# Kernel tuning notes

Hardware: AMD Instinct MI355X
Metric: run time of the kernel (lower is better)

Reference implementation:

```python
import jax, jax.numpy as jnp
import numpy as np

NCHW = ('NCHW', 'OIHW', 'NCHW')


def _conv3x3_same(x, w, b):
    # ZeroPad2d(1) + 3x3 valid conv == 3x3 conv with padding 1
    y = jax.lax.conv_general_dilated(x, w, window_strides=(1, 1),
                                     padding=((1, 1), (1, 1)),
                                     dimension_numbers=NCHW)
    return y + b[None, :, None, None]


def _maxpool2(x):
    return jax.lax.reduce_window(x, -jnp.inf, jax.lax.max,
                                 (1, 1, 2, 2), (1, 1, 2, 2), 'VALID')


def setup_inputs() -> dict:
    key = jax.random.key(0)
    ks = jax.random.split(key, 12)
    B, T1, T2, R, D = 1, 512, 512, 9, 3840
    q = jax.random.normal(ks[0], (B, T1, R, D), jnp.float32)
    t = jax.random.normal(ks[1], (B, T2, R, D), jnp.float32)
    # ViSiL features are L2-normalized region descriptors -> sims in [-1,1]
    q = q / jnp.linalg.norm(q, axis=-1, keepdims=True)
    t = t / jnp.linalg.norm(t, axis=-1, keepdims=True)
    s = 0.05
    return {
        'query': q, 'target': t,
        'w1': jax.random.normal(ks[2], (32, 1, 3, 3), jnp.float32) * s,
        'b1': jax.random.normal(ks[3], (32,), jnp.float32) * s,
        'w2': jax.random.normal(ks[4], (64, 32, 3, 3), jnp.float32) * s,
        'b2': jax.random.normal(ks[5], (64,), jnp.float32) * s,
        'w3': jax.random.normal(ks[6], (128, 64, 3, 3), jnp.float32) * s,
        'b3': jax.random.normal(ks[7], (128,), jnp.float32) * s,
        'wf': jax.random.normal(ks[8], (1, 128, 1, 1), jnp.float32) * s,
        'bf': jax.random.normal(ks[9], (1,), jnp.float32) * s,
    }


def reference(query, target, w1, b1, w2, b2, w3, b3, wf, bf):
    # frame-to-frame: region-pair similarity [B,T1,O,P,T2]
    sim5 = jnp.einsum('biok,bjpk->biopj', query, target)
    # Chamfer (axes=[3,2]): max over target regions P, mean over query regions O
    f2f = jnp.mean(jnp.max(sim5, axis=3), axis=2)  # [B,T1,T2]
    # video comperator CNN
    x = f2f[:, None]                                 # [B,1,T1,T2]
    x = _maxpool2(jax.nn.relu(_conv3x3_same(x, w1, b1)))
    x = _maxpool2(jax.nn.relu(_conv3x3_same(x, w2, b2)))
    x = jax.nn.relu(_conv3x3_same(x, w3, b3))
    x = jax.lax.conv_general_dilated(x, wf, (1, 1), ((0, 0), (0, 0)),
                                     dimension_numbers=NCHW)
    x = x + bf[None, :, None, None]
    s = jnp.clip(x[:, 0], -1.0, 1.0)                 # Hardtanh, [B,H,W]
    # video-to-video Chamfer (axes=[2,1]): max over axis 2, mean over axis 1
    return jnp.mean(jnp.max(s, axis=2), axis=1)      # [B]
```

## Files before the change

### kernel.cpp

```cpp
#include <hip/hip_runtime.h>
#include <hip/hip_bf16.h>

typedef float f32x4 __attribute__((ext_vector_type(4)));
typedef int v8i __attribute__((ext_vector_type(8)));

#define AS3 __attribute__((address_space(3)))
#define AS1 __attribute__((address_space(1)))

__global__ __launch_bounds__(256) void cvt_fp8_kernel(const float* __restrict__ q,
                                                      const float* __restrict__ t,
                                                      unsigned int* __restrict__ qd,
                                                      unsigned int* __restrict__ td) {
  int b = blockIdx.x;
  const float4* s4;
  unsigned int* dst;
  int base;
  if (b < 4320) { s4 = (const float4*)q; dst = qd; base = b * 1024; }
  else          { s4 = (const float4*)t; dst = td; base = (b - 4320) * 1024; }
#pragma unroll
  for (int i = 0; i < 4; ++i) {
    int j = base + i * 256 + threadIdx.x;
    float4 v = s4[j];
    int w = 0;
    w = __builtin_amdgcn_cvt_pk_fp8_f32(v.x * 16.f, v.y * 16.f, w, false);
    w = __builtin_amdgcn_cvt_pk_fp8_f32(v.z * 16.f, v.w * 16.f, w, true);
    dst[j] = w;
  }
}

__global__ __launch_bounds__(768) void gemm_cmax_kernel(const unsigned char* __restrict__ qf8,
                                                        const unsigned char* __restrict__ tf8,
                                                        float* __restrict__ f2f) {
  __shared__ __align__(16) char smem[147456];
  const int tid  = threadIdx.x;
  const int wv   = tid >> 6;
  const int lane = tid & 63;
  const int quad = lane >> 4;
  const int l16  = lane & 15;
  const int wrow = wv >> 1, wcol = wv & 1;
  const int x = blockIdx.x & 7, r = blockIdx.x >> 3;
  const int bi = (x >> 1) * 4 + (r & 3);
  const int bj = (x & 1) * 8 + (r >> 2);

  f32x4 acc[3][9];
#pragma unroll
  for (int a = 0; a < 3; ++a)
#pragma unroll
    for (int b = 0; b < 9; ++b) acc[a][b] = (f32x4){0.f, 0.f, 0.f, 0.f};

  const unsigned char* gptr[6];
#pragma unroll
  for (int i = 0; i < 6; ++i) {
    int s   = i * 768 + wv * 64 + lane;
    int mat = (s >= 2304);
    int sm  = s - mat * 2304;
    int row = sm >> 3, pc = sm & 7;
    int gc  = pc ^ (row & 7);
    const unsigned char* base = mat ? (tf8 + (size_t)(bj * 288 + row) * 3840)
                                    : (qf8 + (size_t)(bi * 288 + row) * 3840);
    gptr[i] = base + gc * 16;
  }

  int buf = 0;
#pragma unroll
  for (int i = 0; i < 6; ++i)
    __builtin_amdgcn_global_load_lds((const AS1 void*)(gptr[i]),
                                     (AS3 void*)(smem + (i * 768 + wv * 64) * 16), 16, 0, 0);

  const int arow0 = wrow * 48 + l16;
  const int bcol0 = wcol * 144 + l16;

  for (int kt = 0; kt < 30; ++kt) {
    __syncthreads();
    if (kt < 29) {
      int nb = buf ^ 1;
#pragma unroll
      for (int i = 0; i < 6; ++i)
        __builtin_amdgcn_global_load_lds((const AS1 void*)(gptr[i] + (kt + 1) * 128),
                                         (AS3 void*)(smem + nb * 73728 + (i * 768 + wv * 64) * 16),
                                         16, 0, 0);
    }
    const char* A = smem + buf * 73728;
    const char* B = A + 36864;

    v8i av[3];
#pragma unroll
    for (int sr = 0; sr < 3; ++sr) {
      int row = arow0 + sr * 16;
      int sw  = row & 7;
      int p0  = (quad * 2) ^ sw, p1 = (quad * 2 + 1) ^ sw;
      int4 lo = *(const int4*)(A + row * 128 + p0 * 16);
      int4 hi = *(const int4*)(A + row * 128 + p1 * 16);
      v8i v;
      v[0] = lo.x; v[1] = lo.y; v[2] = lo.z; v[3] = lo.w;
      v[4] = hi.x; v[5] = hi.y; v[6] = hi.z; v[7] = hi.w;
      av[sr] = v;
    }
#pragma unroll
    for (int c = 0; c < 9; ++c) {
      int col = bcol0 + c * 16;
      int sw  = col & 7;
      int p0  = (quad * 2) ^ sw, p1 = (quad * 2 + 1) ^ sw;
      int4 lo = *(const int4*)(B + col * 128 + p0 * 16);
      int4 hi = *(const int4*)(B + col * 128 + p1 * 16);
      v8i bv;
      bv[0] = lo.x; bv[1] = lo.y; bv[2] = lo.z; bv[3] = lo.w;
      bv[4] = hi.x; bv[5] = hi.y; bv[6] = hi.z; bv[7] = hi.w;
      acc[0][c] = __builtin_amdgcn_mfma_scale_f32_16x16x128_f8f6f4(
          av[0], bv, acc[0][c], 0, 0, 0, 0x7f7f7f7f, 0, 0x7f7f7f7f);
      acc[1][c] = __builtin_amdgcn_mfma_scale_f32_16x16x128_f8f6f4(
          av[1], bv, acc[1][c], 0, 0, 0, 0x7f7f7f7f, 0, 0x7f7f7f7f);
      acc[2][c] = __builtin_amdgcn_mfma_scale_f32_16x16x128_f8f6f4(
          av[2], bv, acc[2][c], 0, 0, 0, 0x7f7f7f7f, 0, 0x7f7f7f7f);
    }
    buf ^= 1;
  }

  __syncthreads();
  float* scr  = (float*)smem;
  float* mbuf = (float*)(smem + 18432);
#pragma unroll
  for (int b = 0; b < 18; ++b) {
    const int bw = b / 3, bs = b - bw * 3;
    if (wrow == bw) {
#pragma unroll
      for (int c = 0; c < 9; ++c)
#pragma unroll
        for (int rr = 0; rr < 4; ++rr)
          scr[(quad * 4 + rr) * 288 + wcol * 144 + c * 16 + l16] = acc[bs][c][rr] * (1.f / 256.f);
    }
    __syncthreads();
    if (tid < 512) {
      int row = tid >> 5, jg = tid & 31;
      const float* p = scr + row * 288 + jg * 9;
      float m = p[0];
#pragma unroll
      for (int k = 1; k < 9; ++k) m = fmaxf(m, p[k]);
      mbuf[(b * 16 + row) * 33 + jg] = m;
    }
    __syncthreads();
  }
  for (int p = tid; p < 1024; p += 768) {
    int il = p >> 5, jg = p & 31;
    const float* mp = mbuf + (il * 9) * 33 + jg;
    float s = 0.f;
#pragma unroll
    for (int o = 0; o < 9; ++o) s += mp[o * 33];
    f2f[(size_t)(bi * 32 + il) * 512 + bj * 32 + jg] = s * (1.f / 9.f);
  }
}

__global__ __launch_bounds__(256) void conv1_kernel(const float* __restrict__ in,
                                                    const float* __restrict__ w1,
                                                    const float* __restrict__ b1,
                                                    float* __restrict__ out) {
  __shared__ float tile[34 * 36];
  __shared__ float wl[320];
  int t = blockIdx.x & 255;
  int chg = blockIdx.x >> 8;
  int ty0 = (t >> 4) * 32, tx0 = (t & 15) * 32;
  int py = threadIdx.x >> 4, px = threadIdx.x & 15;

  for (int idx = threadIdx.x; idx < 320; idx += 256)
    wl[idx] = (idx < 288) ? w1[idx] : b1[idx - 288];
  for (int idx = threadIdx.x; idx < 34 * 34; idx += 256) {
    int r = idx / 34, c = idx % 34;
    int gy = ty0 + r - 1, gx = tx0 + c - 1;
    tile[r * 36 + c] = ((unsigned)gy < 512u && (unsigned)gx < 512u) ? in[gy * 512 + gx] : 0.f;
  }
  __syncthreads();

  float win[4][4];
#pragma unroll
  for (int r = 0; r < 4; ++r)
#pragma unroll
    for (int c = 0; c < 4; ++c)
      win[r][c] = tile[(2 * py + r) * 36 + 2 * px + c];

  int gy2 = (t >> 4) * 16 + py, gx2 = (t & 15) * 16 + px;
  int ch0 = chg * 8;
  for (int ch = ch0; ch < ch0 + 8; ++ch) {
    float w[9];
#pragma unroll
    for (int k = 0; k < 9; ++k) w[k] = wl[ch * 9 + k];
    float m = -INFINITY;
#pragma unroll
    for (int a = 0; a < 2; ++a)
#pragma unroll
      for (int b = 0; b < 2; ++b) {
        float s = 0.f;
#pragma unroll
        for (int ky = 0; ky < 3; ++ky)
#pragma unroll
          for (int kx = 0; kx < 3; ++kx) s += win[a + ky][b + kx] * w[ky * 3 + kx];
        m = fmaxf(m, s);
      }
    out[ch * 65536 + gy2 * 256 + gx2] = fmaxf(m + wl[288 + ch], 0.f);
  }
}

__global__ __launch_bounds__(256) void conv2_kernel(const float* __restrict__ in,
                                                    const float* __restrict__ w2,
                                                    const float* __restrict__ b2,
                                                    float* __restrict__ out) {
  __shared__ __align__(16) float wlds[32 * 4 * 12];
  __shared__ __align__(16) float tile[2 * 2 * 10 * 264];
  const int tid = threadIdx.x;
  const int stripe = blockIdx.x & 31, cog = blockIdx.x >> 5;
  const int X = tid;
  const int Y0 = stripe * 8;

  for (int idx = tid; idx < 1152; idx += 256) {
    int co = idx / 288, rem = idx % 288, ci = rem / 9, k = rem % 9;
    wlds[(ci * 4 + co) * 12 + k] = w2[((cog * 4 + co) * 32 + ci) * 9 + k];
  }
  if (tid < 80) {
    int bu = tid / 40, rem = tid % 40, pl = rem / 20, r2 = rem % 20;
    int rr = r2 >> 1, side = r2 & 1;
    tile[bu * 5280 + pl * 2640 + rr * 264 + (side ? 260 : 3)] = 0.f;
  }
  int gof[5], lof[5];
#pragma unroll
  for (int i = 0; i < 5; ++i) {
    int idx = tid + i * 256;
    int rw = idx >> 6, c4 = idx & 63;
    int pl = (rw >= 10), rr = rw - pl * 10;
    int gy = Y0 + rr - 1;
    lof[i] = pl * 2640 + rr * 264 + 4 + c4 * 4;
    gof[i] = ((unsigned)gy < 256u) ? (pl * 65536 + gy * 256 + c4 * 4) : -1;
  }
#pragma unroll
  for (int i = 0; i < 5; ++i) {
    float4 v = (gof[i] >= 0) ? *(const float4*)(in + gof[i]) : (float4){0, 0, 0, 0};
    *(float4*)&tile[lof[i]] = v;
  }
  __syncthreads();

  float acc[8][4];
#pragma unroll
  for (int y = 0; y < 8; ++y)
#pragma unroll
    for (int co = 0; co < 4; ++co) acc[y][co] = 0.f;

#pragma unroll 1
  for (int cb = 0; cb < 16; ++cb) {
    int buf = cb & 1;
    float4 pf[5];
    if (cb < 15) {
#pragma unroll
      for (int i = 0; i < 5; ++i)
        pf[i] = (gof[i] >= 0) ? *(const float4*)(in + gof[i] + (cb + 1) * 131072)
                              : (float4){0, 0, 0, 0};
    }
    const float* tb = tile + buf * 5280;
#pragma unroll
    for (int pl = 0; pl < 2; ++pl) {
      const float* tp = tb + pl * 2640;
      int ci = cb * 2 + pl;
      float w[4][9];
#pragma unroll
      for (int co = 0; co < 4; ++co) {
        const float* wp = &wlds[(ci * 4 + co) * 12];
        float4 w0 = *(const float4*)wp;
        float4 w1 = *(const float4*)(wp + 4);
        w[co][0] = w0.x; w[co][1] = w0.y; w[co][2] = w0.z; w[co][3] = w0.w;
        w[co][4] = w1.x; w[co][5] = w1.y; w[co][6] = w1.z; w[co][7] = w1.w;
        w[co][8] = wp[8];
      }
      float r0[3], r1[3], r2[3];
      const float* p0 = tp + X + 3;
      r0[0] = p0[0]; r0[1] = p0[1]; r0[2] = p0[2];
      const float* p1 = tp + 264 + X + 3;
      r1[0] = p1[0]; r1[1] = p1[1]; r1[2] = p1[2];
#pragma unroll
      for (int y = 0; y < 8; ++y) {
        const float* p2 = tp + (y + 2) * 264 + X + 3;
        r2[0] = p2[0]; r2[1] = p2[1]; r2[2] = p2[2];
#pragma unroll
        for (int co = 0; co < 4; ++co)
          acc[y][co] += r0[0] * w[co][0] + r0[1] * w[co][1] + r0[2] * w[co][2]
                      + r1[0] * w[co][3] + r1[1] * w[co][4] + r1[2] * w[co][5]
                      + r2[0] * w[co][6] + r2[1] * w[co][7] + r2[2] * w[co][8];
        r0[0] = r1[0]; r0[1] = r1[1]; r0[2] = r1[2];
        r1[0] = r2[0]; r1[1] = r2[1]; r1[2] = r2[2];
      }
    }
    if (cb < 15) {
#pragma unroll
      for (int i = 0; i < 5; ++i)
        *(float4*)&tile[(buf ^ 1) * 5280 + lof[i]] = pf[i];
    }
    __syncthreads();
  }

  int x2 = X >> 1;
#pragma unroll
  for (int co = 0; co < 4; ++co) {
    float bias = b2[cog * 4 + co];
#pragma unroll
    for (int y2 = 0; y2 < 4; ++y2) {
      float v = fmaxf(acc[2 * y2][co], acc[2 * y2 + 1][co]);
      v = fmaxf(v + bias, 0.f);
      float o = fmaxf(v, __shfl_xor(v, 1, 64));
      if ((X & 1) == 0)
        out[(cog * 4 + co) * 16384 + (stripe * 4 + y2) * 128 + x2] = o;
    }
  }
}

__global__ __launch_bounds__(256) void conv3_kernel(const float* __restrict__ in,
                                                    const float* __restrict__ w3,
                                                    const float* __restrict__ b3,
                                                    float* __restrict__ out) {
  __shared__ __align__(16) float wlds[64 * 2 * 12];
  __shared__ __align__(16) float tile[2 * 2 * 18 * 136];
  const int tid = threadIdx.x;
  const int stripe = blockIdx.x & 7, cog = blockIdx.x >> 3;
  const int X = tid & 127, yh = tid >> 7;
  const int Y0 = stripe * 16;

  for (int idx = tid; idx < 1152; idx += 256) {
    int co = idx / 576, rem = idx % 576, ci = rem / 9, k = rem % 9;
    wlds[(ci * 2 + co) * 12 + k] = w3[((cog * 2 + co) * 64 + ci) * 9 + k];
  }
  if (tid < 144) {
    int bu = tid / 72, rem = tid % 72, pl = rem / 36, r2 = rem % 36;
    int rr = r2 >> 1, side = r2 & 1;
    tile[bu * 4896 + pl * 2448 + rr * 136 + (side ? 132 : 3)] = 0.f;
  }
  int gof[5], lof[5];
#pragma unroll
  for (int i = 0; i < 5; ++i) {
    int idx = tid + i * 256;
    if (idx < 1152) {
      int rw = idx >> 5, c4 = idx & 31;
      int pl = (rw >= 18), rr = rw - pl * 18;
      int gy = Y0 + rr - 1;
      lof[i] = pl * 2448 + rr * 136 + 4 + c4 * 4;
      gof[i] = ((unsigned)gy < 128u) ? (pl * 16384 + gy * 128 + c4 * 4) : -1;
    } else { lof[i] = -1; gof[i] = -1; }
  }
#pragma unroll
  for (int i = 0; i < 5; ++i)
    if (lof[i] >= 0) {
      float4 v = (gof[i] >= 0) ? *(const float4*)(in + gof[i]) : (float4){0, 0, 0, 0};
      *(float4*)&tile[lof[i]] = v;
    }
  __syncthreads();

  float acc[8][2];
#pragma unroll
  for (int y = 0; y < 8; ++y)
#pragma unroll
    for (int co = 0; co < 2; ++co) acc[y][co] = 0.f;

#pragma unroll 1
  for (int cb = 0; cb < 32; ++cb) {
    int buf = cb & 1;
    float4 pf[5];
    if (cb < 31) {
#pragma unroll
      for (int i = 0; i < 5; ++i)
        pf[i] = (gof[i] >= 0) ? *(const float4*)(in + gof[i] + (cb + 1) * 32768)
                              : (float4){0, 0, 0, 0};
    }
    const float* tb = tile + buf * 4896;
#pragma unroll
    for (int pl = 0; pl < 2; ++pl) {
      const float* tp = tb + pl * 2448;
      int ci = cb * 2 + pl;
      float w[2][9];
#pragma unroll
      for (int co = 0; co < 2; ++co) {
        const float* wp = &wlds[(ci * 2 + co) * 12];
        float4 w0 = *(const float4*)wp;
        float4 w1 = *(const float4*)(wp + 4);
        w[co][0] = w0.x; w[co][1] = w0.y; w[co][2] = w0.z; w[co][3] = w0.w;
        w[co][4] = w1.x; w[co][5] = w1.y; w[co][6] = w1.z; w[co][7] = w1.w;
        w[co][8] = wp[8];
      }
      float r0[3], r1[3], r2[3];
      const float* p0 = tp + (yh * 8) * 136 + X + 3;
      r0[0] = p0[0]; r0[1] = p0[1]; r0[2] = p0[2];
      const float* p1 = tp + (yh * 8 + 1) * 136 + X + 3;
      r1[0] = p1[0]; r1[1] = p1[1]; r1[2] = p1[2];
#pragma unroll
      for (int y = 0; y < 8; ++y) {
        const float* p2 = tp + (yh * 8 + y + 2) * 136 + X + 3;
        r2[0] = p2[0]; r2[1] = p2[1]; r2[2] = p2[2];
#pragma unroll
        for (int co = 0; co < 2; ++co)
          acc[y][co] += r0[0] * w[co][0] + r0[1] * w[co][1] + r0[2] * w[co][2]
                      + r1[0] * w[co][3] + r1[1] * w[co][4] + r1[2] * w[co][5]
                      + r2[0] * w[co][6] + r2[1] * w[co][7] + r2[2] * w[co][8];
        r0[0] = r1[0]; r0[1] = r1[1]; r0[2] = r1[2];
        r1[0] = r2[0]; r1[1] = r2[1]; r1[2] = r2[2];
      }
    }
    if (cb < 31) {
#pragma unroll
      for (int i = 0; i < 5; ++i)
        if (lof[i] >= 0) *(float4*)&tile[(buf ^ 1) * 4896 + lof[i]] = pf[i];
    }
    __syncthreads();
  }

#pragma unroll
  for (int co = 0; co < 2; ++co) {
    float bias = b3[cog * 2 + co];
    float* op = out + (cog * 2 + co) * 16384 + (Y0 + yh * 8) * 128 + X;
#pragma unroll
    for (int y = 0; y < 8; ++y)
      op[y * 128] = fmaxf(acc[y][co] + bias, 0.f);
  }
}

__global__ __launch_bounds__(512) void convf_kernel(const float* __restrict__ in,
                                                    const float* __restrict__ wf,
                                                    const float* __restrict__ bfp,
                                                    float* __restrict__ rowm) {
  __shared__ float part[512];
  int y = blockIdx.x, tid = threadIdx.x;
  int pt = tid >> 7, x = tid & 127;
  float acc = 0.f;
  const float* ip = in + y * 128 + x;
  for (int ci = pt * 32; ci < pt * 32 + 32; ++ci) acc += ip[ci * 16384] * wf[ci];
  part[tid] = acc;
  __syncthreads();
  if (tid < 128) {
    float s = part[tid] + part[tid + 128] + part[tid + 256] + part[tid + 384] + bfp[0];
    part[tid] = fminf(fmaxf(s, -1.f), 1.f);
  }
  __syncthreads();
  if (tid < 64) {
    float m = fmaxf(part[tid], part[tid + 64]);
    for (int off = 32; off; off >>= 1) m = fmaxf(m, __shfl_down(m, off, 64));
    if (tid == 0) rowm[y] = m;
  }
}

__global__ __launch_bounds__(128) void final_kernel(const float* __restrict__ rowm,
                                                    float* __restrict__ out) {
  int x = threadIdx.x;
  float v = rowm[x];
  for (int off = 32; off; off >>= 1) v += __shfl_down(v, off, 64);
  __shared__ float red[2];
  if ((x & 63) == 0) red[x >> 6] = v;
  __syncthreads();
  if (x == 0) out[0] = (red[0] + red[1]) * (1.f / 128.f);
}

extern "C" void kernel_launch(void* const* d_in, const int* in_sizes, int n_in,
                              void* d_out, int out_size, void* d_ws, size_t ws_size,
                              hipStream_t stream) {
  const float* q  = (const float*)d_in[0];
  const float* t  = (const float*)d_in[1];
  const float* w1 = (const float*)d_in[2];
  const float* b1 = (const float*)d_in[3];
  const float* w2 = (const float*)d_in[4];
  const float* b2 = (const float*)d_in[5];
  const float* w3 = (const float*)d_in[6];
  const float* b3 = (const float*)d_in[7];
  const float* wf = (const float*)d_in[8];
  const float* bf = (const float*)d_in[9];
  float* out = (float*)d_out;
  char* ws = (char*)d_ws;

  unsigned char* qf8 = (unsigned char*)(ws + 0);
  unsigned char* tf8 = (unsigned char*)(ws + 17694720);
  float* f2f  = (float*)(ws + 44826624);
  float* x1   = (float*)(ws + 45875200);
  float* x2b  = (float*)(ws + 54263808);
  float* x3   = (float*)(ws + 58458112);
  float* rowm = (float*)(ws + 66846720);

  cvt_fp8_kernel<<<8640, 256, 0, stream>>>(q, t, (unsigned int*)qf8, (unsigned int*)tf8);
  gemm_cmax_kernel<<<256, 768, 0, stream>>>(qf8, tf8, f2f);
  conv1_kernel<<<1024, 256, 0, stream>>>(f2f, w1, b1, x1);
  conv2_kernel<<<512, 256, 0, stream>>>(x1, w2, b2, x2b);
  conv3_kernel<<<512, 256, 0, stream>>>(x2b, w3, b3, x3);
  convf_kernel<<<128, 512, 0, stream>>>(x3, wf, bf, rowm);
  final_kernel<<<1, 128, 0, stream>>>(rowm, out);
}
```

Before: 384.4 us.

## Fuse conv stages into one persistent kernel with grid barriers

Replaces the five separate conv/reduction kernel launches with a single 512-block kernel that runs conv1, conv2, conv3, the 1x1 conv and the final reduction in sequence. Stages are separated by atomic-counter grid barriers, and the counters are reset with a memset before each run. The goal is to remove launch gaps and tail effects between the small conv kernels. The cost is spin-wait barrier overhead, and it relies on all 512 blocks being co-resident, which holds given the shared-memory and thread usage on this GPU.

```diff
diff --git a/kernel.cpp b/kernel.cpp
--- a/kernel.cpp
+++ b/kernel.cpp
@@ -150,304 +150,325 @@
   }
 }
 
-__global__ __launch_bounds__(256) void conv1_kernel(const float* __restrict__ in,
-                                                    const float* __restrict__ w1,
-                                                    const float* __restrict__ b1,
-                                                    float* __restrict__ out) {
-  __shared__ float tile[34 * 36];
-  __shared__ float wl[320];
-  int t = blockIdx.x & 255;
-  int chg = blockIdx.x >> 8;
-  int ty0 = (t >> 4) * 32, tx0 = (t & 15) * 32;
-  int py = threadIdx.x >> 4, px = threadIdx.x & 15;
-
-  for (int idx = threadIdx.x; idx < 320; idx += 256)
-    wl[idx] = (idx < 288) ? w1[idx] : b1[idx - 288];
-  for (int idx = threadIdx.x; idx < 34 * 34; idx += 256) {
-    int r = idx / 34, c = idx % 34;
-    int gy = ty0 + r - 1, gx = tx0 + c - 1;
-    tile[r * 36 + c] = ((unsigned)gy < 512u && (unsigned)gx < 512u) ? in[gy * 512 + gx] : 0.f;
-  }
+__device__ __forceinline__ void grid_barrier(unsigned int* cnt, unsigned int nb) {
   __syncthreads();
-
-  float win[4][4];
-#pragma unroll
-  for (int r = 0; r < 4; ++r)
-#pragma unroll
-    for (int c = 0; c < 4; ++c)
-      win[r][c] = tile[(2 * py + r) * 36 + 2 * px + c];
-
-  int gy2 = (t >> 4) * 16 + py, gx2 = (t & 15) * 16 + px;
-  int ch0 = chg * 8;
-  for (int ch = ch0; ch < ch0 + 8; ++ch) {
-    float w[9];
-#pragma unroll
-    for (int k = 0; k < 9; ++k) w[k] = wl[ch * 9 + k];
-    float m = -INFINITY;
-#pragma unroll
-    for (int a = 0; a < 2; ++a)
-#pragma unroll
-      for (int b = 0; b < 2; ++b) {
-        float s = 0.f;
-#pragma unroll
-        for (int ky = 0; ky < 3; ++ky)
-#pragma unroll
-          for (int kx = 0; kx < 3; ++kx) s += win[a + ky][b + kx] * w[ky * 3 + kx];
-        m = fmaxf(m, s);
-      }
-    out[ch * 65536 + gy2 * 256 + gx2] = fmaxf(m + wl[288 + ch], 0.f);
-  }
+  if (threadIdx.x == 0) {
+    __threadfence();
+    atomicAdd(cnt, 1u);
+    while (atomicAdd(cnt, 0u) < nb) __builtin_amdgcn_s_sleep(8);
+    __threadfence();
+  }
+  __syncthreads();
 }
 
-__global__ __launch_bounds__(256) void conv2_kernel(const float* __restrict__ in,
-                                                    const float* __restrict__ w2,
-                                                    const float* __restrict__ b2,
-                                                    float* __restrict__ out) {
-  __shared__ __align__(16) float wlds[32 * 4 * 12];
-  __shared__ __align__(16) float tile[2 * 2 * 10 * 264];
+__global__ __launch_bounds__(256) void megaconv_kernel(const float* __restrict__ f2f,
+                                                       const float* __restrict__ w1,
+                                                       const float* __restrict__ b1,
+                                                       const float* __restrict__ w2,
+                                                       const float* __restrict__ b2,
+                                                       const float* __restrict__ w3,
+                                                       const float* __restrict__ b3,
+                                                       const float* __restrict__ wf,
+                                                       const float* __restrict__ bfp,
+                                                       float* __restrict__ x1,
+                                                       float* __restrict__ x2b,
+                                                       float* __restrict__ x3,
+                                                       float* __restrict__ rowm,
+                                                       unsigned int* __restrict__ bars,
+                                                       float* __restrict__ out) {
+  __shared__ __align__(16) char pool[48384];
+  const int b = blockIdx.x;
   const int tid = threadIdx.x;
-  const int stripe = blockIdx.x & 31, cog = blockIdx.x >> 5;
-  const int X = tid;
-  const int Y0 = stripe * 8;
-
-  for (int idx = tid; idx < 1152; idx += 256) {
-    int co = idx / 288, rem = idx % 288, ci = rem / 9, k = rem % 9;
-    wlds[(ci * 4 + co) * 12 + k] = w2[((cog * 4 + co) * 32 + ci) * 9 + k];
-  }
-  if (tid < 80) {
-    int bu = tid / 40, rem = tid % 40, pl = rem / 20, r2 = rem % 20;
-    int rr = r2 >> 1, side = r2 & 1;
-    tile[bu * 5280 + pl * 2640 + rr * 264 + (side ? 260 : 3)] = 0.f;
-  }
-  int gof[5], lof[5];
-#pragma unroll
-  for (int i = 0; i < 5; ++i) {
-    int idx = tid + i * 256;
-    int rw = idx >> 6, c4 = idx & 63;
-    int pl = (rw >= 10), rr = rw - pl * 10;
-    int gy = Y0 + rr - 1;
-    lof[i] = pl * 2640 + rr * 264 + 4 + c4 * 4;
-    gof[i] = ((unsigned)gy < 256u) ? (pl * 65536 + gy * 256 + c4 * 4) : -1;
-  }
-#pragma unroll
-  for (int i = 0; i < 5; ++i) {
-    float4 v = (gof[i] >= 0) ? *(const float4*)(in + gof[i]) : (float4){0, 0, 0, 0};
-    *(float4*)&tile[lof[i]] = v;
-  }
-  __syncthreads();
-
-  float acc[8][4];
-#pragma unroll
-  for (int y = 0; y < 8; ++y)
-#pragma unroll
-    for (int co = 0; co < 4; ++co) acc[y][co] = 0.f;
-
+
+  {
+    float* wl = (float*)pool;
+    float* tile1 = (float*)(pool + 1280);
+    int t = b & 255;
+    int ty0 = (t >> 4) * 32, tx0 = (t & 15) * 32;
+    int py = tid >> 4, px = tid & 15;
+
+    for (int idx = tid; idx < 320; idx += 256)
+      wl[idx] = (idx < 288) ? w1[idx] : b1[idx - 288];
+    for (int idx = tid; idx < 34 * 34; idx += 256) {
+      int rr = idx / 34, cc = idx % 34;
+      int gy = ty0 + rr - 1, gx = tx0 + cc - 1;
+      tile1[rr * 36 + cc] = ((unsigned)gy < 512u && (unsigned)gx < 512u) ? f2f[gy * 512 + gx] : 0.f;
+    }
+    __syncthreads();
+
+    float win[4][4];
+#pragma unroll
+    for (int rr = 0; rr < 4; ++rr)
+#pragma unroll
+      for (int cc = 0; cc < 4; ++cc)
+        win[rr][cc] = tile1[(2 * py + rr) * 36 + 2 * px + cc];
+
+    int gy2 = (t >> 4) * 16 + py, gx2 = (t & 15) * 16 + px;
 #pragma unroll 1
-  for (int cb = 0; cb < 16; ++cb) {
-    int buf = cb & 1;
-    float4 pf[5];
-    if (cb < 15) {
-#pragma unroll
-      for (int i = 0; i < 5; ++i)
-        pf[i] = (gof[i] >= 0) ? *(const float4*)(in + gof[i] + (cb + 1) * 131072)
-                              : (float4){0, 0, 0, 0};
-    }
-    const float* tb = tile + buf * 5280;
-#pragma unroll
-    for (int pl = 0; pl < 2; ++pl) {
-      const float* tp = tb + pl * 2640;
-      int ci = cb * 2 + pl;
-      float w[4][9];
-#pragma unroll
-      for (int co = 0; co < 4; ++co) {
-        const float* wp = &wlds[(ci * 4 + co) * 12];
-        float4 w0 = *(const float4*)wp;
-        float4 w1 = *(const float4*)(wp + 4);
-        w[co][0] = w0.x; w[co][1] = w0.y; w[co][2] = w0.z; w[co][3] = w0.w;
-        w[co][4] = w1.x; w[co][5] = w1.y; w[co][6] = w1.z; w[co][7] = w1.w;
-        w[co][8] = wp[8];
-      }
-      float r0[3], r1[3], r2[3];
-      const float* p0 = tp + X + 3;
-      r0[0] = p0[0]; r0[1] = p0[1]; r0[2] = p0[2];
-      const float* p1 = tp + 264 + X + 3;
-      r1[0] = p1[0]; r1[1] = p1[1]; r1[2] = p1[2];
-#pragma unroll
-      for (int y = 0; y < 8; ++y) {
-        const float* p2 = tp + (y + 2) * 264 + X + 3;
-        r2[0] = p2[0]; r2[1] = p2[1]; r2[2] = p2[2];
-#pragma unroll
-        for (int co = 0; co < 4; ++co)
-          acc[y][co] += r0[0] * w[co][0] + r0[1] * w[co][1] + r0[2] * w[co][2]
-                      + r1[0] * w[co][3] + r1[1] * w[co][4] + r1[2] * w[co][5]
-                      + r2[0] * w[co][6] + r2[1] * w[co][7] + r2[2] * w[co][8];
-        r0[0] = r1[0]; r0[1] = r1[1]; r0[2] = r1[2];
-        r1[0] = r2[0]; r1[1] = r2[1]; r1[2] = r2[2];
-      }
-    }
-    if (cb < 15) {
-#pragma unroll
-      for (int i = 0; i < 5; ++i)
-        *(float4*)&tile[(buf ^ 1) * 5280 + lof[i]] = pf[i];
-    }
-    __syncthreads();
-  }
-
-  int x2 = X >> 1;
-#pragma unroll
-  for (int co = 0; co < 4; ++co) {
-    float bias = b2[cog * 4 + co];
-#pragma unroll
-    for (int y2 = 0; y2 < 4; ++y2) {
-      float v = fmaxf(acc[2 * y2][co], acc[2 * y2 + 1][co]);
-      v = fmaxf(v + bias, 0.f);
-      float o = fmaxf(v, __shfl_xor(v, 1, 64));
-      if ((X & 1) == 0)
-        out[(cog * 4 + co) * 16384 + (stripe * 4 + y2) * 128 + x2] = o;
-    }
-  }
-}
-
-__global__ __launch_bounds__(256) void conv3_kernel(const float* __restrict__ in,
-                                                    const float* __restrict__ w3,
-                                                    const float* __restrict__ b3,
-                                                    float* __restrict__ out) {
-  __shared__ __align__(16) float wlds[64 * 2 * 12];
-  __shared__ __align__(16) float tile[2 * 2 * 18 * 136];
-  const int tid = threadIdx.x;
-  const int stripe = blockIdx.x & 7, cog = blockIdx.x >> 3;
-  const int X = tid & 127, yh = tid >> 7;
-  const int Y0 = stripe * 16;
-
-  for (int idx = tid; idx < 1152; idx += 256) {
-    int co = idx / 576, rem = idx % 576, ci = rem / 9, k = rem % 9;
-    wlds[(ci * 2 + co) * 12 + k] = w3[((cog * 2 + co) * 64 + ci) * 9 + k];
-  }
-  if (tid < 144) {
-    int bu = tid / 72, rem = tid % 72, pl = rem / 36, r2 = rem % 36;
-    int rr = r2 >> 1, side = r2 & 1;
-    tile[bu * 4896 + pl * 2448 + rr * 136 + (side ? 132 : 3)] = 0.f;
-  }
-  int gof[5], lof[5];
-#pragma unroll
-  for (int i = 0; i < 5; ++i) {
-    int idx = tid + i * 256;
-    if (idx < 1152) {
-      int rw = idx >> 5, c4 = idx & 31;
-      int pl = (rw >= 18), rr = rw - pl * 18;
+    for (int g = 0; g < 2; ++g) {
+      int ch0 = ((b >> 8) + g * 2) * 8;
+      for (int ch = ch0; ch < ch0 + 8; ++ch) {
+        float w[9];
+#pragma unroll
+        for (int k = 0; k < 9; ++k) w[k] = wl[ch * 9 + k];
+        float m = -INFINITY;
+#pragma unroll
+        for (int a = 0; a < 2; ++a)
+#pragma unroll
+          for (int bb = 0; bb < 2; ++bb) {
+            float s = 0.f;
+#pragma unroll
+            for (int ky = 0; ky < 3; ++ky)
+#pragma unroll
+              for (int kx = 0; kx < 3; ++kx) s += win[a + ky][bb + kx] * w[ky * 3 + kx];
+            m = fmaxf(m, s);
+          }
+        x1[ch * 65536 + gy2 * 256 + gx2] = fmaxf(m + wl[288 + ch], 0.f);
+      }
+    }
+  }
+  grid_barrier(bars + 0, 512);
+
+  {
+    float* wlds = (float*)pool;
+    float* tile = (float*)(pool + 6144);
+    const int stripe = b & 31, cog = b >> 5;
+    const int X = tid;
+    const int Y0 = stripe * 8;
+
+    for (int idx = tid; idx < 1152; idx += 256) {
+      int co = idx / 288, rem = idx % 288, ci = rem / 9, k = rem % 9;
+      wlds[(ci * 4 + co) * 12 + k] = w2[((cog * 4 + co) * 32 + ci) * 9 + k];
+    }
+    if (tid < 80) {
+      int bu = tid / 40, rem = tid % 40, pl = rem / 20, r2 = rem % 20;
+      int rr = r2 >> 1, side = r2 & 1;
+      tile[bu * 5280 + pl * 2640 + rr * 264 + (side ? 260 : 3)] = 0.f;
+    }
+    int gof[5], lof[5];
+#pragma unroll
+    for (int i = 0; i < 5; ++i) {
+      int idx = tid + i * 256;
+      int rw = idx >> 6, c4 = idx & 63;
+      int pl = (rw >= 10), rr = rw - pl * 10;
       int gy = Y0 + rr - 1;
-      lof[i] = pl * 2448 + rr * 136 + 4 + c4 * 4;
-      gof[i] = ((unsigned)gy < 128u) ? (pl * 16384 + gy * 128 + c4 * 4) : -1;
-    } else { lof[i] = -1; gof[i] = -1; }
-  }
-#pragma unroll
-  for (int i = 0; i < 5; ++i)
-    if (lof[i] >= 0) {
-      float4 v = (gof[i] >= 0) ? *(const float4*)(in + gof[i]) : (float4){0, 0, 0, 0};
+      lof[i] = pl * 2640 + rr * 264 + 4 + c4 * 4;
+      gof[i] = ((unsigned)gy < 256u) ? (pl * 65536 + gy * 256 + c4 * 4) : -1;
+    }
+#pragma unroll
+    for (int i = 0; i < 5; ++i) {
+      float4 v = (gof[i] >= 0) ? *(const float4*)(x1 + gof[i]) : (float4){0, 0, 0, 0};
       *(float4*)&tile[lof[i]] = v;
     }
-  __syncthreads();
-
-  float acc[8][2];
-#pragma unroll
-  for (int y = 0; y < 8; ++y)
-#pragma unroll
-    for (int co = 0; co < 2; ++co) acc[y][co] = 0.f;
+    __syncthreads();
+
+    float acc[8][4];
+#pragma unroll
+    for (int y = 0; y < 8; ++y)
+#pragma unroll
+      for (int co = 0; co < 4; ++co) acc[y][co] = 0.f;
 
 #pragma unroll 1
-  for (int cb = 0; cb < 32; ++cb) {
-    int buf = cb & 1;
-    float4 pf[5];
-    if (cb < 31) {
-#pragma unroll
-      for (int i = 0; i < 5; ++i)
-        pf[i] = (gof[i] >= 0) ? *(const float4*)(in + gof[i] + (cb + 1) * 32768)
-                              : (float4){0, 0, 0, 0};
-    }
-    const float* tb = tile + buf * 4896;
-#pragma unroll
-    for (int pl = 0; pl < 2; ++pl) {
-      const float* tp = tb + pl * 2448;
-      int ci = cb * 2 + pl;
-      float w[2][9];
-#pragma unroll
-      for (int co = 0; co < 2; ++co) {
-        const float* wp = &wlds[(ci * 2 + co) * 12];
-        float4 w0 = *(const float4*)wp;
-        float4 w1 = *(const float4*)(wp + 4);
-        w[co][0] = w0.x; w[co][1] = w0.y; w[co][2] = w0.z; w[co][3] = w0.w;
-        w[co][4] = w1.x; w[co][5] = w1.y; w[co][6] = w1.z; w[co][7] = w1.w;
-        w[co][8] = wp[8];
-      }
-      float r0[3], r1[3], r2[3];
-      const float* p0 = tp + (yh * 8) * 136 + X + 3;
-      r0[0] = p0[0]; r0[1] = p0[1]; r0[2] = p0[2];
-      const float* p1 = tp + (yh * 8 + 1) * 136 + X + 3;
-      r1[0] = p1[0]; r1[1] = p1[1]; r1[2] = p1[2];
-#pragma unroll
-      for (int y = 0; y < 8; ++y) {
-        const float* p2 = tp + (yh * 8 + y + 2) * 136 + X + 3;
-        r2[0] = p2[0]; r2[1] = p2[1]; r2[2] = p2[2];
-#pragma unroll
-        for (int co = 0; co < 2; ++co)
-          acc[y][co] += r0[0] * w[co][0] + r0[1] * w[co][1] + r0[2] * w[co][2]
-                      + r1[0] * w[co][3] + r1[1] * w[co][4] + r1[2] * w[co][5]
-                      + r2[0] * w[co][6] + r2[1] * w[co][7] + r2[2] * w[co][8];
-        r0[0] = r1[0]; r0[1] = r1[1]; r0[2] = r1[2];
-        r1[0] = r2[0]; r1[1] = r2[1]; r1[2] = r2[2];
-      }
-    }
-    if (cb < 31) {
-#pragma unroll
-      for (int i = 0; i < 5; ++i)
-        if (lof[i] >= 0) *(float4*)&tile[(buf ^ 1) * 4896 + lof[i]] = pf[i];
-    }
-    __syncthreads();
-  }
-
-#pragma unroll
-  for (int co = 0; co < 2; ++co) {
-    float bias = b3[cog * 2 + co];
-    float* op = out + (cog * 2 + co) * 16384 + (Y0 + yh * 8) * 128 + X;
+    for (int cb = 0; cb < 16; ++cb) {
+      int buf = cb & 1;
+      float4 pf[5];
+      if (cb < 15) {
+#pragma unroll
+        for (int i = 0; i < 5; ++i)
+          pf[i] = (gof[i] >= 0) ? *(const float4*)(x1 + gof[i] + (cb + 1) * 131072)
+                                : (float4){0, 0, 0, 0};
+      }
+      const float* tb = tile + buf * 5280;
+#pragma unroll
+      for (int pl = 0; pl < 2; ++pl) {
+        const float* tp = tb + pl * 2640;
+        int ci = cb * 2 + pl;
+        float w[4][9];
+#pragma unroll
+        for (int co = 0; co < 4; ++co) {
+          const float* wp = &wlds[(ci * 4 + co) * 12];
+          float4 w0 = *(const float4*)wp;
+          float4 w1v = *(const float4*)(wp + 4);
+          w[co][0] = w0.x; w[co][1] = w0.y; w[co][2] = w0.z; w[co][3] = w0.w;
+          w[co][4] = w1v.x; w[co][5] = w1v.y; w[co][6] = w1v.z; w[co][7] = w1v.w;
+          w[co][8] = wp[8];
+        }
+        float r0[3], r1[3], r2[3];
+        const float* p0 = tp + X + 3;
+        r0[0] = p0[0]; r0[1] = p0[1]; r0[2] = p0[2];
+        const float* p1 = tp + 264 + X + 3;
+        r1[0] = p1[0]; r1[1] = p1[1]; r1[2] = p1[2];
+#pragma unroll
+        for (int y = 0; y < 8; ++y) {
+          const float* p2 = tp + (y + 2) * 264 + X + 3;
+          r2[0] = p2[0]; r2[1] = p2[1]; r2[2] = p2[2];
+#pragma unroll
+          for (int co = 0; co < 4; ++co)
+            acc[y][co] += r0[0] * w[co][0] + r0[1] * w[co][1] + r0[2] * w[co][2]
+                        + r1[0] * w[co][3] + r1[1] * w[co][4] + r1[2] * w[co][5]
+                        + r2[0] * w[co][6] + r2[1] * w[co][7] + r2[2] * w[co][8];
+          r0[0] = r1[0]; r0[1] = r1[1]; r0[2] = r1[2];
+          r1[0] = r2[0]; r1[1] = r2[1]; r1[2] = r2[2];
+        }
+      }
+      if (cb < 15) {
+#pragma unroll
+        for (int i = 0; i < 5; ++i)
+          *(float4*)&tile[(buf ^ 1) * 5280 + lof[i]] = pf[i];
+      }
+      __syncthreads();
+    }
+
+    int x2 = X >> 1;
+#pragma unroll
+    for (int co = 0; co < 4; ++co) {
+      float bias = b2[cog * 4 + co];
+#pragma unroll
+      for (int y2 = 0; y2 < 4; ++y2) {
+        float v = fmaxf(acc[2 * y2][co], acc[2 * y2 + 1][co]);
+        v = fmaxf(v + bias, 0.f);
+        float o = fmaxf(v, __shfl_xor(v, 1, 64));
+        if ((X & 1) == 0)
+          x2b[(cog * 4 + co) * 16384 + (stripe * 4 + y2) * 128 + x2] = o;
+      }
+    }
+  }
+  grid_barrier(bars + 1, 512);
+
+  {
+    float* wlds = (float*)pool;
+    float* tile = (float*)(pool + 6144);
+    const int stripe = b & 7, cog = b >> 3;
+    const int X = tid & 127, yh = tid >> 7;
+    const int Y0 = stripe * 16;
+
+    for (int idx = tid; idx < 1152; idx += 256) {
+      int co = idx / 576, rem = idx % 576, ci = rem / 9, k = rem % 9;
+      wlds[(ci * 2 + co) * 12 + k] = w3[((cog * 2 + co) * 64 + ci) * 9 + k];
+    }
+    if (tid < 144) {
+      int bu = tid / 72, rem = tid % 72, pl = rem / 36, r2 = rem % 36;
+      int rr = r2 >> 1, side = r2 & 1;
+      tile[bu * 4896 + pl * 2448 + rr * 136 + (side ? 132 : 3)] = 0.f;
+    }
+    int gof[5], lof[5];
+#pragma unroll
+    for (int i = 0; i < 5; ++i) {
+      int idx = tid + i * 256;
+      if (idx < 1152) {
+        int rw = idx >> 5, c4 = idx & 31;
+        int pl = (rw >= 18), rr = rw - pl * 18;
+        int gy = Y0 + rr - 1;
+        lof[i] = pl * 2448 + rr * 136 + 4 + c4 * 4;
+        gof[i] = ((unsigned)gy < 128u) ? (pl * 16384 + gy * 128 + c4 * 4) : -1;
+      } else { lof[i] = -1; gof[i] = -1; }
+    }
+#pragma unroll
+    for (int i = 0; i < 5; ++i)
+      if (lof[i] >= 0) {
+        float4 v = (gof[i] >= 0) ? *(const float4*)(x2b + gof[i]) : (float4){0, 0, 0, 0};
+        *(float4*)&tile[lof[i]] = v;
+      }
+    __syncthreads();
+
+    float acc[8][2];
 #pragma unroll
     for (int y = 0; y < 8; ++y)
-      op[y * 128] = fmaxf(acc[y][co] + bias, 0.f);
-  }
-}
-
-__global__ __launch_bounds__(512) void convf_kernel(const float* __restrict__ in,
-                                                    const float* __restrict__ wf,
-                                                    const float* __restrict__ bfp,
-                                                    float* __restrict__ rowm) {
-  __shared__ float part[512];
-  int y = blockIdx.x, tid = threadIdx.x;
-  int pt = tid >> 7, x = tid & 127;
-  float acc = 0.f;
-  const float* ip = in + y * 128 + x;
-  for (int ci = pt * 32; ci < pt * 32 + 32; ++ci) acc += ip[ci * 16384] * wf[ci];
-  part[tid] = acc;
-  __syncthreads();
-  if (tid < 128) {
-    float s = part[tid] + part[tid + 128] + part[tid + 256] + part[tid + 384] + bfp[0];
-    part[tid] = fminf(fmaxf(s, -1.f), 1.f);
-  }
-  __syncthreads();
-  if (tid < 64) {
-    float m = fmaxf(part[tid], part[tid + 64]);
-    for (int off = 32; off; off >>= 1) m = fmaxf(m, __shfl_down(m, off, 64));
-    if (tid == 0) rowm[y] = m;
-  }
-}
-
-__global__ __launch_bounds__(128) void final_kernel(const float* __restrict__ rowm,
-                                                    float* __restrict__ out) {
-  int x = threadIdx.x;
-  float v = rowm[x];
-  for (int off = 32; off; off >>= 1) v += __shfl_down(v, off, 64);
-  __shared__ float red[2];
-  if ((x & 63) == 0) red[x >> 6] = v;
-  __syncthreads();
-  if (x == 0) out[0] = (red[0] + red[1]) * (1.f / 128.f);
+#pragma unroll
+      for (int co = 0; co < 2; ++co) acc[y][co] = 0.f;
+
+#pragma unroll 1
+    for (int cb = 0; cb < 32; ++cb) {
+      int buf = cb & 1;
+      float4 pf[5];
+      if (cb < 31) {
+#pragma unroll
+        for (int i = 0; i < 5; ++i)
+          pf[i] = (gof[i] >= 0) ? *(const float4*)(x2b + gof[i] + (cb + 1) * 32768)
+                                : (float4){0, 0, 0, 0};
+      }
+      const float* tb = tile + buf * 4896;
+#pragma unroll
+      for (int pl = 0; pl < 2; ++pl) {
+        const float* tp = tb + pl * 2448;
+        int ci = cb * 2 + pl;
+        float w[2][9];
+#pragma unroll
+        for (int co = 0; co < 2; ++co) {
+          const float* wp = &wlds[(ci * 2 + co) * 12];
+          float4 w0 = *(const float4*)wp;
+          float4 w1v = *(const float4*)(wp + 4);
+          w[co][0] = w0.x; w[co][1] = w0.y; w[co][2] = w0.z; w[co][3] = w0.w;
+          w[co][4] = w1v.x; w[co][5] = w1v.y; w[co][6] = w1v.z; w[co][7] = w1v.w;
+          w[co][8] = wp[8];
+        }
+        float r0[3], r1[3], r2[3];
+        const float* p0 = tp + (yh * 8) * 136 + X + 3;
+        r0[0] = p0[0]; r0[1] = p0[1]; r0[2] = p0[2];
+        const float* p1 = tp + (yh * 8 + 1) * 136 + X + 3;
+        r1[0] = p1[0]; r1[1] = p1[1]; r1[2] = p1[2];
+#pragma unroll
+        for (int y = 0; y < 8; ++y) {
+          const float* p2 = tp + (yh * 8 + y + 2) * 136 + X + 3;
+          r2[0] = p2[0]; r2[1] = p2[1]; r2[2] = p2[2];
+#pragma unroll
+          for (int co = 0; co < 2; ++co)
+            acc[y][co] += r0[0] * w[co][0] + r0[1] * w[co][1] + r0[2] * w[co][2]
+                        + r1[0] * w[co][3] + r1[1] * w[co][4] + r1[2] * w[co][5]
+                        + r2[0] * w[co][6] + r2[1] * w[co][7] + r2[2] * w[co][8];
+          r0[0] = r1[0]; r0[1] = r1[1]; r0[2] = r1[2];
+          r1[0] = r2[0]; r1[1] = r2[1]; r1[2] = r2[2];
+        }
+      }
+      if (cb < 31) {
+#pragma unroll
+        for (int i = 0; i < 5; ++i)
+          if (lof[i] >= 0) *(float4*)&tile[(buf ^ 1) * 4896 + lof[i]] = pf[i];
+      }
+      __syncthreads();
+    }
+
+#pragma unroll
+    for (int co = 0; co < 2; ++co) {
+      float bias = b3[cog * 2 + co];
+      float* op = x3 + (cog * 2 + co) * 16384 + (Y0 + yh * 8) * 128 + X;
+#pragma unroll
+      for (int y = 0; y < 8; ++y)
+        op[y * 128] = fmaxf(acc[y][co] + bias, 0.f);
+    }
+  }
+  grid_barrier(bars + 2, 512);
+
+  if (b < 128) {
+    float* fpart = (float*)pool;
+    int y = b;
+    int xx = tid & 127, pt = tid >> 7;
+    float acc = 0.f;
+    const float* ip = x3 + y * 128 + xx;
+    for (int ci = pt * 64; ci < pt * 64 + 64; ++ci) acc += ip[ci * 16384] * wf[ci];
+    fpart[tid] = acc;
+    __syncthreads();
+    if (tid < 128) {
+      float s = fpart[tid] + fpart[tid + 128] + bfp[0];
+      fpart[tid] = fminf(fmaxf(s, -1.f), 1.f);
+    }
+    __syncthreads();
+    if (tid < 64) {
+      float m = fmaxf(fpart[tid], fpart[tid + 64]);
+      for (int off = 32; off; off >>= 1) m = fmaxf(m, __shfl_down(m, off, 64));
+      if (tid == 0) rowm[y] = m;
+    }
+  }
+  grid_barrier(bars + 3, 512);
+
+  if (b == 0) {
+    float* red = (float*)pool;
+    float v = (tid < 128) ? rowm[tid] : 0.f;
+    for (int off = 32; off; off >>= 1) v += __shfl_down(v, off, 64);
+    if (tid < 128 && (tid & 63) == 0) red[tid >> 6] = v;
+    __syncthreads();
+    if (tid == 0) out[0] = (red[0] + red[1]) * (1.f / 128.f);
+  }
 }
 
 extern "C" void kernel_launch(void* const* d_in, const int* in_sizes, int n_in,
@@ -473,12 +494,11 @@
   float* x2b  = (float*)(ws + 54263808);
   float* x3   = (float*)(ws + 58458112);
   float* rowm = (float*)(ws + 66846720);
-
+  unsigned int* bars = (unsigned int*)(ws + 66847232);
+
+  hipMemsetAsync(bars, 0, 64, stream);
   cvt_fp8_kernel<<<8640, 256, 0, stream>>>(q, t, (unsigned int*)qf8, (unsigned int*)tf8);
   gemm_cmax_kernel<<<256, 768, 0, stream>>>(qf8, tf8, f2f);
-  conv1_kernel<<<1024, 256, 0, stream>>>(f2f, w1, b1, x1);
-  conv2_kernel<<<512, 256, 0, stream>>>(x1, w2, b2, x2b);
-  conv3_kernel<<<512, 256, 0, stream>>>(x2b, w3, b3, x3);
-  convf_kernel<<<128, 512, 0, stream>>>(x3, wf, bf, rowm);
-  final_kernel<<<1, 128, 0, stream>>>(rowm, out);
+  megaconv_kernel<<<512, 256, 0, stream>>>(f2f, w1, b1, w2, b2, w3, b3, wf, bf,
+                                           x1, x2b, x3, rowm, bars, out);
 }
```

Measured after the change: 545.8 us. +42.0%, slower.

## Fuse conv3, final 1x1 conv and reduction via grid barrier

Applied to the files above, without the earlier changes.

Merges conv3, the 1x1 conv with row-max, and the final mean into one kernel. After conv3 a device-wide atomic barrier waits for all 512 blocks, then 128 blocks compute the row maxima and the last block to finish does the mean. This removes two kernel launches and their gaps, at the cost of an added memset and a spin barrier. The barrier assumes all 512 blocks are resident at once; if they are not, the kernel deadlocks.

```diff
diff --git a/kernel.cpp b/kernel.cpp
--- a/kernel.cpp
+++ b/kernel.cpp
@@ -262,9 +262,9 @@
       for (int co = 0; co < 4; ++co) {
         const float* wp = &wlds[(ci * 4 + co) * 12];
         float4 w0 = *(const float4*)wp;
-        float4 w1 = *(const float4*)(wp + 4);
+        float4 w1v = *(const float4*)(wp + 4);
         w[co][0] = w0.x; w[co][1] = w0.y; w[co][2] = w0.z; w[co][3] = w0.w;
-        w[co][4] = w1.x; w[co][5] = w1.y; w[co][6] = w1.z; w[co][7] = w1.w;
+        w[co][4] = w1v.x; w[co][5] = w1v.y; w[co][6] = w1v.z; w[co][7] = w1v.w;
         w[co][8] = wp[8];
       }
       float r0[3], r1[3], r2[3];
@@ -308,14 +308,21 @@
   }
 }
 
-__global__ __launch_bounds__(256) void conv3_kernel(const float* __restrict__ in,
-                                                    const float* __restrict__ w3,
-                                                    const float* __restrict__ b3,
-                                                    float* __restrict__ out) {
+__global__ __launch_bounds__(256) void conv3f_kernel(const float* __restrict__ in,
+                                                     const float* __restrict__ w3,
+                                                     const float* __restrict__ b3,
+                                                     const float* __restrict__ wf,
+                                                     const float* __restrict__ bfp,
+                                                     float* __restrict__ x3,
+                                                     float* __restrict__ rowm,
+                                                     unsigned int* __restrict__ bars,
+                                                     float* __restrict__ out) {
   __shared__ __align__(16) float wlds[64 * 2 * 12];
   __shared__ __align__(16) float tile[2 * 2 * 18 * 136];
+  __shared__ unsigned int lastf;
+  const int b = blockIdx.x;
   const int tid = threadIdx.x;
-  const int stripe = blockIdx.x & 7, cog = blockIdx.x >> 3;
+  const int stripe = b & 7, cog = b >> 3;
   const int X = tid & 127, yh = tid >> 7;
   const int Y0 = stripe * 16;
 
@@ -374,9 +381,9 @@
       for (int co = 0; co < 2; ++co) {
         const float* wp = &wlds[(ci * 2 + co) * 12];
         float4 w0 = *(const float4*)wp;
-        float4 w1 = *(const float4*)(wp + 4);
+        float4 w1v = *(const float4*)(wp + 4);
         w[co][0] = w0.x; w[co][1] = w0.y; w[co][2] = w0.z; w[co][3] = w0.w;
-        w[co][4] = w1.x; w[co][5] = w1.y; w[co][6] = w1.z; w[co][7] = w1.w;
+        w[co][4] = w1v.x; w[co][5] = w1v.y; w[co][6] = w1v.z; w[co][7] = w1v.w;
         w[co][8] = wp[8];
       }
       float r0[3], r1[3], r2[3];
@@ -408,46 +415,59 @@
 #pragma unroll
   for (int co = 0; co < 2; ++co) {
     float bias = b3[cog * 2 + co];
-    float* op = out + (cog * 2 + co) * 16384 + (Y0 + yh * 8) * 128 + X;
+    float* op = x3 + (cog * 2 + co) * 16384 + (Y0 + yh * 8) * 128 + X;
 #pragma unroll
     for (int y = 0; y < 8; ++y)
       op[y * 128] = fmaxf(acc[y][co] + bias, 0.f);
   }
-}
-
-__global__ __launch_bounds__(512) void convf_kernel(const float* __restrict__ in,
-                                                    const float* __restrict__ wf,
-                                                    const float* __restrict__ bfp,
-                                                    float* __restrict__ rowm) {
-  __shared__ float part[512];
-  int y = blockIdx.x, tid = threadIdx.x;
-  int pt = tid >> 7, x = tid & 127;
-  float acc = 0.f;
-  const float* ip = in + y * 128 + x;
-  for (int ci = pt * 32; ci < pt * 32 + 32; ++ci) acc += ip[ci * 16384] * wf[ci];
-  part[tid] = acc;
+
   __syncthreads();
-  if (tid < 128) {
-    float s = part[tid] + part[tid + 128] + part[tid + 256] + part[tid + 384] + bfp[0];
-    part[tid] = fminf(fmaxf(s, -1.f), 1.f);
+  if (tid == 0) {
+    __threadfence();
+    __hip_atomic_fetch_add(bars + 0, 1u, __ATOMIC_ACQ_REL, __HIP_MEMORY_SCOPE_AGENT);
+    while (__hip_atomic_load(bars + 0, __ATOMIC_ACQUIRE, __HIP_MEMORY_SCOPE_AGENT) < 512u)
+      __builtin_amdgcn_s_sleep(32);
+    __threadfence();
   }
   __syncthreads();
-  if (tid < 64) {
-    float m = fmaxf(part[tid], part[tid + 64]);
-    for (int off = 32; off; off >>= 1) m = fmaxf(m, __shfl_down(m, off, 64));
-    if (tid == 0) rowm[y] = m;
-  }
-}
-
-__global__ __launch_bounds__(128) void final_kernel(const float* __restrict__ rowm,
-                                                    float* __restrict__ out) {
-  int x = threadIdx.x;
-  float v = rowm[x];
-  for (int off = 32; off; off >>= 1) v += __shfl_down(v, off, 64);
-  __shared__ float red[2];
-  if ((x & 63) == 0) red[x >> 6] = v;
-  __syncthreads();
-  if (x == 0) out[0] = (red[0] + red[1]) * (1.f / 128.f);
+
+  if (b < 128) {
+    float* fpart = wlds;
+    int y = b;
+    int pt = tid >> 7;
+    float facc = 0.f;
+    const float* ip = x3 + y * 128 + X;
+    for (int ci = pt * 64; ci < pt * 64 + 64; ++ci) facc += ip[ci * 16384] * wf[ci];
+    fpart[tid] = facc;
+    __syncthreads();
+    if (tid < 128) {
+      float s = fpart[tid] + fpart[tid + 128] + bfp[0];
+      fpart[tid] = fminf(fmaxf(s, -1.f), 1.f);
+    }
+    __syncthreads();
+    if (tid < 64) {
+      float m = fmaxf(fpart[tid], fpart[tid + 64]);
+      for (int off = 32; off; off >>= 1) m = fmaxf(m, __shfl_down(m, off, 64));
+      if (tid == 0) rowm[y] = m;
+    }
+    __syncthreads();
+    if (tid == 0) {
+      __threadfence();
+      unsigned int old = __hip_atomic_fetch_add(bars + 1, 1u, __ATOMIC_ACQ_REL,
+                                                __HIP_MEMORY_SCOPE_AGENT);
+      lastf = (old == 127u) ? 1u : 0u;
+      if (lastf) __threadfence();
+    }
+    __syncthreads();
+    if (lastf) {
+      float* red = wlds;
+      float v = (tid < 128) ? rowm[tid] : 0.f;
+      for (int off = 32; off; off >>= 1) v += __shfl_down(v, off, 64);
+      if (tid < 128 && (tid & 63) == 0) red[tid >> 6] = v;
+      __syncthreads();
+      if (tid == 0) out[0] = (red[0] + red[1]) * (1.f / 128.f);
+    }
+  }
 }
 
 extern "C" void kernel_launch(void* const* d_in, const int* in_sizes, int n_in,
@@ -473,12 +493,12 @@
   float* x2b  = (float*)(ws + 54263808);
   float* x3   = (float*)(ws + 58458112);
   float* rowm = (float*)(ws + 66846720);
-
+  unsigned int* bars = (unsigned int*)(ws + 66847232);
+
+  hipMemsetAsync(bars, 0, 16, stream);
   cvt_fp8_kernel<<<8640, 256, 0, stream>>>(q, t, (unsigned int*)qf8, (unsigned int*)tf8);
   gemm_cmax_kernel<<<256, 768, 0, stream>>>(qf8, tf8, f2f);
   conv1_kernel<<<1024, 256, 0, stream>>>(f2f, w1, b1, x1);
   conv2_kernel<<<512, 256, 0, stream>>>(x1, w2, b2, x2b);
-  conv3_kernel<<<512, 256, 0, stream>>>(x2b, w3, b3, x3);
-  convf_kernel<<<128, 512, 0, stream>>>(x3, wf, bf, rowm);
-  final_kernel<<<1, 128, 0, stream>>>(rowm, out);
+  conv3f_kernel<<<512, 256, 0, stream>>>(x2b, w3, b3, wf, bf, x3, rowm, bars, out);
 }
```

Result: slower. 462.2 us (+20.2%).
